# Optimization experiments

Measured on AMD Instinct MI355X. Metric: run time of the kernel, lower is better.

Reference implementation:

```python
import jax, jax.numpy as jnp
import numpy as np
import math

N = 100000   # outputSize (memory bank rows)
D = 128      # inputSize (feature dim)
B = 128      # batch size
K = 4096     # number of negatives per sample
T = 0.07     # temperature
MOMENTUM = 0.5


def setup_inputs() -> dict:
    key = jax.random.key(0)
    k1, k2, k3, k4, k5 = jax.random.split(key, 5)
    stdv = 1.0 / math.sqrt(D / 3.0)
    # l2-normalized features, as produced by the encoder in contrastive setups
    v1 = jax.random.normal(k1, (B, D), dtype=jnp.float32)
    v1 = v1 / jnp.linalg.norm(v1, axis=1, keepdims=True)
    v2 = jax.random.normal(k2, (B, D), dtype=jnp.float32)
    v2 = v2 / jnp.linalg.norm(v2, axis=1, keepdims=True)
    idx = jax.random.randint(k3, (B, K + 1), 0, N, dtype=jnp.int32)  # pos+neg bank rows
    y = jnp.arange(B, dtype=jnp.int32)  # distinct positive slots (first-visit behavior)
    # memory buffers initialized U(-stdv, stdv), as in torch.rand*2*stdv - stdv
    memory_v1 = jax.random.uniform(k4, (N, D), dtype=jnp.float32, minval=-stdv, maxval=stdv)
    memory_v2 = jax.random.uniform(k5, (N, D), dtype=jnp.float32, minval=-stdv, maxval=stdv)
    return {"v1": v1, "v2": v2, "idx": idx, "y": y,
            "memory_v1": memory_v1, "memory_v2": memory_v2}


def reference(v1, v2, idx, y, memory_v1, memory_v2):
    n_out = memory_v1.shape[0]
    # gather K+1 rows per sample (detached in the original -> stop_gradient)
    w1 = jax.lax.stop_gradient(memory_v1[idx])  # [B, K+1, D]
    w2 = jax.lax.stop_gradient(memory_v2[idx])  # [B, K+1, D]
    # batched vector-matrix product + exp/T
    out_v2 = jnp.exp(jnp.einsum('bkd,bd->bk', w1, v2) / T)  # [B, K+1]
    out_v1 = jnp.exp(jnp.einsum('bkd,bd->bk', w2, v1) / T)  # [B, K+1]
    # normalization constants (first-call Z computation: mean * outputSize)
    Z_v1 = jax.lax.stop_gradient(out_v1.mean()) * n_out
    Z_v2 = jax.lax.stop_gradient(out_v2.mean()) * n_out
    out_v1 = out_v1 / Z_v1
    out_v2 = out_v2 / Z_v2
    # momentum-blended normalize-and-scatter memory update (no_grad in torch)
    upd1 = MOMENTUM * memory_v1[y] + (1.0 - MOMENTUM) * v1  # [B, D]
    upd1 = upd1 / jnp.linalg.norm(upd1, axis=1, keepdims=True)
    new_memory_v1 = memory_v1.at[y].set(upd1)
    upd2 = MOMENTUM * memory_v2[y] + (1.0 - MOMENTUM) * v2
    upd2 = upd2 / jnp.linalg.norm(upd2, axis=1, keepdims=True)
    new_memory_v2 = memory_v2.at[y].set(upd2)
    return out_v1, out_v2, new_memory_v1, new_memory_v2
```

## Files before the change

### kernel.cpp

```cpp
#include <hip/hip_runtime.h>
#include <math.h>

constexpr int N_ROWS = 100000;
constexpr int D      = 128;
constexpr int B      = 128;
constexpr int KP1    = 4097;
constexpr int TOTAL_PAIRS = B * KP1;
constexpr float INV_T = 1.0f / 0.07f;
constexpr int N4 = N_ROWS * (D / 4);

constexpr int SC_BLOCKS = 1024;
constexpr int CP_BLOCKS = 1024;

__global__ void init_ws_kernel(float* ws) {
    if (threadIdx.x < 2) ws[threadIdx.x] = 0.0f;
}

__device__ __forceinline__ float dot4(float4 a, float4 b) {
    return a.x * b.x + a.y * b.y + a.z * b.z + a.w * b.w;
}

__device__ __forceinline__ float red32(float v) {
    #pragma unroll
    for (int off = 16; off >= 1; off >>= 1) v += __shfl_xor(v, off);
    return v;
}

__global__ __launch_bounds__(256) void mega_kernel(
    const float* __restrict__ v1, const float* __restrict__ v2,
    const int* __restrict__ idx,
    const float* __restrict__ mem1, const float* __restrict__ mem2,
    float* __restrict__ out,
    float* __restrict__ sums,
    float4* __restrict__ o1, float4* __restrict__ o2)
{
    if (blockIdx.x & 1) {
        int cid = blockIdx.x >> 1;
        const float4* __restrict__ m1 = (const float4*)mem1;
        const float4* __restrict__ m2 = (const float4*)mem2;
        int tid = cid * 256 + threadIdx.x;
        int stride = CP_BLOCKS * 256;
        for (int i = tid; i < N4; i += stride) {
            o1[i] = m1[i];
            o2[i] = m2[i];
        }
        return;
    }

    const int sid = blockIdx.x >> 1;
    const int l   = threadIdx.x & 31;
    const int grp = threadIdx.x >> 5;
    const int g   = sid * 8 + grp;
    const int b   = g >> 6;
    const int gk  = g & 63;

    const float4* __restrict__ m1 = (const float4*)mem1;
    const float4* __restrict__ m2 = (const float4*)mem2;
    const float4 a1 = ((const float4*)v1)[b * 32 + l];
    const float4 a2 = ((const float4*)v2)[b * 32 + l];
    const int base = b * KP1;

    float acc1 = 0.0f, acc2 = 0.0f;
    int k = gk;
    for (; k + 64 < KP1; k += 128) {
        int p0 = base + k, p1 = base + k + 64;
        int r0 = idx[p0], r1 = idx[p1];
        float4 w10 = m1[(size_t)r0 * 32 + l];
        float4 w20 = m2[(size_t)r0 * 32 + l];
        float4 w11 = m1[(size_t)r1 * 32 + l];
        float4 w21 = m2[(size_t)r1 * 32 + l];

        float d10 = red32(dot4(w20, a1));
        float d20 = red32(dot4(w10, a2));
        float d11 = red32(dot4(w21, a1));
        float d21 = red32(dot4(w11, a2));

        if (l == 0) {
            float e10 = __expf(d10 * INV_T);
            float e20 = __expf(d20 * INV_T);
            float e11 = __expf(d11 * INV_T);
            float e21 = __expf(d21 * INV_T);
            out[p0]               = e10;
            out[TOTAL_PAIRS + p0] = e20;
            out[p1]               = e11;
            out[TOTAL_PAIRS + p1] = e21;
            acc1 += e10 + e11;
            acc2 += e20 + e21;
        }
    }
    for (; k < KP1; k += 64) {
        int p0 = base + k;
        int r0 = idx[p0];
        float4 w10 = m1[(size_t)r0 * 32 + l];
        float4 w20 = m2[(size_t)r0 * 32 + l];
        float d10 = red32(dot4(w20, a1));
        float d20 = red32(dot4(w10, a2));
        if (l == 0) {
            float e10 = __expf(d10 * INV_T);
            float e20 = __expf(d20 * INV_T);
            out[p0]               = e10;
            out[TOTAL_PAIRS + p0] = e20;
            acc1 += e10;
            acc2 += e20;
        }
    }

    __shared__ float s1[8], s2[8];
    if (l == 0) { s1[grp] = acc1; s2[grp] = acc2; }
    __syncthreads();
    if (threadIdx.x == 0) {
        float t1 = 0.0f, t2 = 0.0f;
        #pragma unroll
        for (int i = 0; i < 8; ++i) { t1 += s1[i]; t2 += s2[i]; }
        atomicAdd(&sums[0], t1);
        atomicAdd(&sums[1], t2);
    }
}

__global__ __launch_bounds__(256) void finish_kernel(
    float* __restrict__ out, const float* __restrict__ sums,
    const float* __restrict__ v1, const float* __restrict__ v2,
    const int* __restrict__ y,
    const float* __restrict__ mem1, const float* __restrict__ mem2,
    float* __restrict__ o1, float* __restrict__ o2)
{
    if (blockIdx.x < 2 * B && threadIdx.x < 64) {
        int b    = blockIdx.x & (B - 1);
        int bank = blockIdx.x >> 7;
        int lane = threadIdx.x;
        const float2* __restrict__ m = (const float2*)(bank ? mem2 : mem1);
        const float2* __restrict__ v = (const float2*)(bank ? v2 : v1);
        float2* __restrict__ o       = (float2*)(bank ? o2 : o1);
        int row = y[b];
        float2 mv = m[(size_t)row * 64 + lane];
        float2 vv = v[b * 64 + lane];
        float2 u;
        u.x = 0.5f * mv.x + 0.5f * vv.x;
        u.y = 0.5f * mv.y + 0.5f * vv.y;
        float ss = u.x * u.x + u.y * u.y;
        #pragma unroll
        for (int off = 32; off >= 1; off >>= 1) ss += __shfl_xor(ss, off);
        float inv = 1.0f / sqrtf(ss);
        float2 r; r.x = u.x * inv; r.y = u.y * inv;
        o[(size_t)row * 64 + lane] = r;
    }

    float sc1 = (float)((double)TOTAL_PAIRS / ((double)sums[0] * (double)N_ROWS));
    float sc2 = (float)((double)TOTAL_PAIRS / ((double)sums[1] * (double)N_ROWS));
    int stride = gridDim.x * blockDim.x;
    for (int i = blockIdx.x * blockDim.x + threadIdx.x; i < 2 * TOTAL_PAIRS;
         i += stride) {
        out[i] *= (i < TOTAL_PAIRS) ? sc1 : sc2;
    }
}

extern "C" void kernel_launch(void* const* d_in, const int* in_sizes, int n_in,
                              void* d_out, int out_size, void* d_ws, size_t ws_size,
                              hipStream_t stream) {
    const float* v1   = (const float*)d_in[0];
    const float* v2   = (const float*)d_in[1];
    const int*   idx  = (const int*)d_in[2];
    const int*   y    = (const int*)d_in[3];
    const float* mem1 = (const float*)d_in[4];
    const float* mem2 = (const float*)d_in[5];

    float* out = (float*)d_out;
    float* out_mem1 = out + 2 * (size_t)TOTAL_PAIRS;
    float* out_mem2 = out_mem1 + (size_t)N_ROWS * D;
    float* sums = (float*)d_ws;

    init_ws_kernel<<<1, 64, 0, stream>>>(sums);

    mega_kernel<<<SC_BLOCKS + CP_BLOCKS, 256, 0, stream>>>(
        v1, v2, idx, mem1, mem2, out, sums,
        (float4*)out_mem1, (float4*)out_mem2);

    finish_kernel<<<1024, 256, 0, stream>>>(
        out, sums, v1, v2, y, mem1, mem2, out_mem1, out_mem2);
}
```

Baseline: 288.5 us.

## Stage indices in LDS, unroll gather by four, nontemporal bank copy

Each score block now owns a contiguous 512-index chunk of one batch row. It stages those indices into shared memory and has each warp process 64 consecutive pairs, issuing eight independent row gathers per iteration for more memory-level parallelism. Outputs are written as four contiguous values by lanes 0-7 instead of scattered single-lane stores. The memory-bank copy half uses nontemporal stores so it does not pollute cache. In exchange it uses more registers, and the odd 4097th element is handled by a tail path.

```diff
diff --git a/kernel.cpp b/kernel.cpp
--- a/kernel.cpp
+++ b/kernel.cpp
@@ -12,6 +12,8 @@
 constexpr int SC_BLOCKS = 1024;
 constexpr int CP_BLOCKS = 1024;
 
+typedef float fvec4 __attribute__((ext_vector_type(4)));
+
 __global__ void init_ws_kernel(float* ws) {
     if (threadIdx.x < 2) ws[threadIdx.x] = 0.0f;
 }
@@ -32,83 +34,113 @@
     const float* __restrict__ mem1, const float* __restrict__ mem2,
     float* __restrict__ out,
     float* __restrict__ sums,
-    float4* __restrict__ o1, float4* __restrict__ o2)
+    float* __restrict__ o1, float* __restrict__ o2)
 {
     if (blockIdx.x & 1) {
         int cid = blockIdx.x >> 1;
-        const float4* __restrict__ m1 = (const float4*)mem1;
-        const float4* __restrict__ m2 = (const float4*)mem2;
+        const fvec4* __restrict__ m1 = (const fvec4*)mem1;
+        const fvec4* __restrict__ m2 = (const fvec4*)mem2;
+        fvec4* __restrict__ d1 = (fvec4*)o1;
+        fvec4* __restrict__ d2 = (fvec4*)o2;
         int tid = cid * 256 + threadIdx.x;
         int stride = CP_BLOCKS * 256;
         for (int i = tid; i < N4; i += stride) {
-            o1[i] = m1[i];
-            o2[i] = m2[i];
+            fvec4 x1 = m1[i];
+            fvec4 x2 = m2[i];
+            __builtin_nontemporal_store(x1, &d1[i]);
+            __builtin_nontemporal_store(x2, &d2[i]);
         }
         return;
     }
 
-    const int sid = blockIdx.x >> 1;
-    const int l   = threadIdx.x & 31;
-    const int grp = threadIdx.x >> 5;
-    const int g   = sid * 8 + grp;
-    const int b   = g >> 6;
-    const int gk  = g & 63;
+    __shared__ alignas(16) int s_idx[516];
+    __shared__ float s1[8], s2[8];
+
+    const int sid   = blockIdx.x >> 1;
+    const int tid   = threadIdx.x;
+    const int l     = tid & 31;
+    const int grp   = tid >> 5;
+    const int b     = sid >> 3;
+    const int chunk = sid & 7;
+    const int cnt   = (chunk == 7) ? 513 : 512;
+    const int ibase = b * KP1 + chunk * 512;
+
+    for (int t = tid; t < cnt; t += 256) s_idx[t] = idx[ibase + t];
+    __syncthreads();
 
     const float4* __restrict__ m1 = (const float4*)mem1;
     const float4* __restrict__ m2 = (const float4*)mem2;
     const float4 a1 = ((const float4*)v1)[b * 32 + l];
     const float4 a2 = ((const float4*)v2)[b * 32 + l];
-    const int base = b * KP1;
+
+    const int lk    = grp * 64;
+    const int pbase = ibase + lk;
 
     float acc1 = 0.0f, acc2 = 0.0f;
-    int k = gk;
-    for (; k + 64 < KP1; k += 128) {
-        int p0 = base + k, p1 = base + k + 64;
-        int r0 = idx[p0], r1 = idx[p1];
-        float4 w10 = m1[(size_t)r0 * 32 + l];
-        float4 w20 = m2[(size_t)r0 * 32 + l];
-        float4 w11 = m1[(size_t)r1 * 32 + l];
-        float4 w21 = m2[(size_t)r1 * 32 + l];
-
-        float d10 = red32(dot4(w20, a1));
-        float d20 = red32(dot4(w10, a2));
-        float d11 = red32(dot4(w21, a1));
-        float d21 = red32(dot4(w11, a2));
-
+
+    for (int u = 0; u < 64; u += 4) {
+        const int4 rr = *(const int4*)&s_idx[lk + u];
+
+        float4 wA0 = m2[(size_t)rr.x * 32 + l];
+        float4 wB0 = m1[(size_t)rr.x * 32 + l];
+        float4 wA1 = m2[(size_t)rr.y * 32 + l];
+        float4 wB1 = m1[(size_t)rr.y * 32 + l];
+        float4 wA2 = m2[(size_t)rr.z * 32 + l];
+        float4 wB2 = m1[(size_t)rr.z * 32 + l];
+        float4 wA3 = m2[(size_t)rr.w * 32 + l];
+        float4 wB3 = m1[(size_t)rr.w * 32 + l];
+
+        float dA0 = red32(dot4(wA0, a1));
+        float dB0 = red32(dot4(wB0, a2));
+        float dA1 = red32(dot4(wA1, a1));
+        float dB1 = red32(dot4(wB1, a2));
+        float dA2 = red32(dot4(wA2, a1));
+        float dB2 = red32(dot4(wB2, a2));
+        float dA3 = red32(dot4(wA3, a1));
+        float dB3 = red32(dot4(wB3, a2));
+
+        float eA0 = __expf(dA0 * INV_T);
+        float eB0 = __expf(dB0 * INV_T);
+        float eA1 = __expf(dA1 * INV_T);
+        float eB1 = __expf(dB1 * INV_T);
+        float eA2 = __expf(dA2 * INV_T);
+        float eB2 = __expf(dB2 * INV_T);
+        float eA3 = __expf(dA3 * INV_T);
+        float eB3 = __expf(dB3 * INV_T);
+
+        acc1 += (eA0 + eA1) + (eA2 + eA3);
+        acc2 += (eB0 + eB1) + (eB2 + eB3);
+
+        float sa  = (l & 1) ? eA1 : eA0;
+        float sb  = (l & 1) ? eA3 : eA2;
+        float evA = (l & 2) ? sb : sa;
+        float sc  = (l & 1) ? eB1 : eB0;
+        float sd  = (l & 1) ? eB3 : eB2;
+        float evB = (l & 2) ? sd : sc;
+        int p = pbase + u;
+        if (l < 4)      out[p + l] = evA;
+        else if (l < 8) out[TOTAL_PAIRS + p + (l - 4)] = evB;
+    }
+
+    if (chunk == 7 && grp == 7) {
+        int r = s_idx[512];
+        float4 wA = m2[(size_t)r * 32 + l];
+        float4 wB = m1[(size_t)r * 32 + l];
+        float dA = red32(dot4(wA, a1));
+        float dB = red32(dot4(wB, a2));
+        float eA = __expf(dA * INV_T);
+        float eB = __expf(dB * INV_T);
+        acc1 += eA;
+        acc2 += eB;
         if (l == 0) {
-            float e10 = __expf(d10 * INV_T);
-            float e20 = __expf(d20 * INV_T);
-            float e11 = __expf(d11 * INV_T);
-            float e21 = __expf(d21 * INV_T);
-            out[p0]               = e10;
-            out[TOTAL_PAIRS + p0] = e20;
-            out[p1]               = e11;
-            out[TOTAL_PAIRS + p1] = e21;
-            acc1 += e10 + e11;
-            acc2 += e20 + e21;
+            out[b * KP1 + 4096]               = eA;
+            out[TOTAL_PAIRS + b * KP1 + 4096] = eB;
         }
     }
-    for (; k < KP1; k += 64) {
-        int p0 = base + k;
-        int r0 = idx[p0];
-        float4 w10 = m1[(size_t)r0 * 32 + l];
-        float4 w20 = m2[(size_t)r0 * 32 + l];
-        float d10 = red32(dot4(w20, a1));
-        float d20 = red32(dot4(w10, a2));
-        if (l == 0) {
-            float e10 = __expf(d10 * INV_T);
-            float e20 = __expf(d20 * INV_T);
-            out[p0]               = e10;
-            out[TOTAL_PAIRS + p0] = e20;
-            acc1 += e10;
-            acc2 += e20;
-        }
-    }
-
-    __shared__ float s1[8], s2[8];
+
     if (l == 0) { s1[grp] = acc1; s2[grp] = acc2; }
     __syncthreads();
-    if (threadIdx.x == 0) {
+    if (tid == 0) {
         float t1 = 0.0f, t2 = 0.0f;
         #pragma unroll
         for (int i = 0; i < 8; ++i) { t1 += s1[i]; t2 += s2[i]; }
@@ -172,8 +204,7 @@
     init_ws_kernel<<<1, 64, 0, stream>>>(sums);
 
     mega_kernel<<<SC_BLOCKS + CP_BLOCKS, 256, 0, stream>>>(
-        v1, v2, idx, mem1, mem2, out, sums,
-        (float4*)out_mem1, (float4*)out_mem2);
+        v1, v2, idx, mem1, mem2, out, sums, out_mem1, out_mem2);
 
     finish_kernel<<<1024, 256, 0, stream>>>(
         out, sums, v1, v2, y, mem1, mem2, out_mem1, out_mem2);
```

Result: faster. 282.7 us (-2.0%).
